# Optimization experiments

Measured on AMD Instinct MI355X. Metric: run time of the kernel, lower is better.

Reference implementation:

```python
import jax, jax.numpy as jnp
import numpy as np
import math

B, S, D, H = 16, 256, 1024, 16
DK = D // H
MAXLEN = 512


def _sinusoid_table(maxlen, dim):
    # rows for positions -maxlen .. maxlen-1  (2*maxlen rows)
    pos = jnp.arange(-maxlen, maxlen, dtype=jnp.float32)[:, None]
    i = jnp.arange(dim)
    angle = pos / jnp.power(10000.0, (2 * (i // 2)) / dim).astype(jnp.float32)
    return jnp.where(i % 2 == 0, jnp.sin(angle), jnp.cos(angle))


def setup_inputs() -> dict:
    key = jax.random.key(0)
    ks = jax.random.split(key, 13)
    std_qk = math.sqrt(2.0 / (D + DK))
    inp = {
        "x": jax.random.normal(ks[0], (B, S, D), jnp.float32),
        "Wq": jax.random.normal(ks[1], (D, D), jnp.float32) * std_qk,
        "bq": jnp.zeros((D,), jnp.float32),
        "Wk": jax.random.normal(ks[2], (D, D), jnp.float32) * std_qk,
        "bk": jnp.zeros((D,), jnp.float32),
        "Wv": jax.random.normal(ks[3], (D, D), jnp.float32) * std_qk,
        "bv": jnp.zeros((D,), jnp.float32),
        "Wr": jax.random.normal(ks[4], (D, D), jnp.float32) * std_qk,
        "br": jnp.zeros((D,), jnp.float32),
        "u_bias": jax.random.normal(ks[5], (H, DK), jnp.float32) * math.sqrt(2.0 / (H + DK)),
        "v_bias": jax.random.normal(ks[6], (H, DK), jnp.float32) * math.sqrt(2.0 / (H + DK)),
        "Wo": jax.random.normal(ks[7], (D, D), jnp.float32) * math.sqrt(2.0 / (D + D)),
        "bo": jnp.zeros((D,), jnp.float32),
    }
    return inp


def reference(x, Wq, bq, Wk, bk, Wv, bv, Wr, br, u_bias, v_bias, Wo, bo):
    table = _sinusoid_table(MAXLEN, D)  # (2*MAXLEN, D)
    # relative position indices: idx[s, z] = z - s, shifted by +MAXLEN
    relpos_idx = (jnp.arange(2 * S)[None, :] - jnp.arange(S)[:, None])[:, :S] + MAXLEN
    relpos_vec = table[relpos_idx]  # (S, S, D)

    q = (x @ Wq.T + bq).reshape(B, S, H, DK)
    k = (x @ Wk.T + bk).reshape(B, S, H, DK)
    v = (x @ Wv.T + bv).reshape(B, S, H, DK)

    rp_k = (relpos_vec @ Wk.T + bk).reshape(S, S, H, DK)       # shared k_proj
    kR = (x @ Wr.T + br).reshape(B, S, H, DK)                  # relpos_k_proj(keys)
    rp_R = (relpos_vec @ Wr.T + br).reshape(S, S, H, DK)       # relpos_k_proj(relpos)

    w = jnp.einsum('bshd,bzhd->bhsz', q, k)
    w = w + jnp.einsum('bshd,szhd->bhsz', q, rp_k)
    w = w + jnp.einsum('hd,bzhd->bhz', u_bias, kR)[:, :, None, :]
    w = w + jnp.einsum('hd,szhd->hsz', v_bias, rp_R)[None, :, :, :]
    w = w / math.sqrt(DK)

    causal = jnp.tril(jnp.ones((S, S), jnp.float32))[None, None, :, :]
    w = w + jnp.log(causal)  # -inf above diagonal

    attn = jax.nn.softmax(w, axis=-1)                          # (B,H,S,S)
    vw = jnp.einsum('bhsz,bzhd->bshd', attn, v).reshape(B, S, D)
    return vw @ Wo.T + bo
```

## Files before the change

### kernel.cpp

```cpp
#include <hip/hip_runtime.h>
#include <math.h>

constexpr int kB  = 16;
constexpr int kS  = 256;
constexpr int kD  = 1024;
constexpr int kH  = 16;
constexpr float kScale = 0.125f;

using bf16x8  = __attribute__((ext_vector_type(8))) short;
using floatx4 = __attribute__((ext_vector_type(4))) float;
typedef unsigned short u16;

__device__ __forceinline__ u16 f2bf(float x) {
  union { float f; unsigned u; } v; v.f = x;
  unsigned r = v.u + 0x7fffu + ((v.u >> 16) & 1u);
  return (u16)(r >> 16);
}
__device__ __forceinline__ float bf2f(u16 h) {
  union { unsigned u; float f; } v; v.u = ((unsigned)h) << 16;
  return v.f;
}

#define MFMA16(a, b, c) __builtin_amdgcn_mfma_f32_16x16x32_bf16((a), (b), (c), 0, 0, 0)
#define GLL16(gp, lp)                                                        \
  __builtin_amdgcn_global_load_lds(                                          \
      (const __attribute__((address_space(1))) unsigned int*)(gp),           \
      (__attribute__((address_space(3))) unsigned int*)(lp), 16, 0, 0)

__global__ __launch_bounds__(256) void pack_k(
    const float* __restrict__ x, const float* __restrict__ Wq,
    const float* __restrict__ Wk, const float* __restrict__ Wv,
    const float* __restrict__ Wo,
    const float* __restrict__ bq, const float* __restrict__ bk,
    const float* __restrict__ bv,
    const float* __restrict__ Wr, const float* __restrict__ br,
    const float* __restrict__ ub, const float* __restrict__ vb,
    u16* __restrict__ xA, u16* __restrict__ W3b, u16* __restrict__ Wob,
    float* __restrict__ b3) {
  if (blockIdx.x >= 8451) {
    int gid = (blockIdx.x - 8451) * 256 + threadIdx.x;
    int j = gid >> 10, c = gid & 1023;
    int h = j & 15;
    const float* bvec = (j < 16 ? ub : vb) + h * 64;
    const float* wcol = Wr + (size_t)(h * 64) * 1024 + c;
    float a = 0.f;
#pragma unroll
    for (int d = 0; d < 64; ++d) a += bvec[d] * wcol[(size_t)d * 1024];
    W3b[(size_t)(3072 + j) * 1024 + c] = f2bf(a);
    if (gid < 128) {
      float s = 0.f;
      if (gid < 32) {
        const float* bv2 = (gid < 16 ? ub : vb) + (gid & 15) * 64;
        const float* brp = br + (gid & 15) * 64;
        for (int d = 0; d < 64; ++d) s += bv2[d] * brp[d];
      }
      b3[3072 + gid] = s;
    }
    return;
  }
  size_t i = ((size_t)blockIdx.x * 256 + threadIdx.x) * 4;
  const size_t NX = (size_t)4194304, NW = (size_t)1048576;
  const size_t BEND = NX + 4 * NW + 3072;
  const float* src;
  u16* dst;
  size_t o;
  if (i < NX) {
    src = x; dst = xA; o = i;
  } else if (i < NX + 3 * NW) {
    size_t j = i - NX;
    int sel = (int)(j >> 20);
    o = j & (NW - 1);
    src = sel == 0 ? Wq : sel == 1 ? Wv : Wk;
    dst = W3b + (size_t)sel * NW;
  } else if (i < NX + 4 * NW) {
    o = i - NX - 3 * NW;
    src = Wo; dst = Wob;
  } else if (i < BEND) {
    size_t j = i - NX - 4 * NW;
    int sel = (int)(j >> 10);
    o = j & 1023;
    src = sel == 0 ? bq : sel == 1 ? bv : bk;
    *reinterpret_cast<float4*>(b3 + j) = *reinterpret_cast<const float4*>(src + o);
    return;
  } else if (i < BEND + 262144) {
    size_t j = i - BEND;
    int p = (int)(j >> 10);
    int ibase = (int)(j & 1023);
    ushort4 r;
    u16* rr = (u16*)&r;
#pragma unroll
    for (int c = 0; c < 4; ++c) {
      int idx = ibase + c;
      float ex = (float)(2 * (idx / 2)) * (1.0f / 1024.0f);
      float scale = exp2f(ex * -13.287712379549449f);
      float angle = (float)(p - 255) * scale;
      rr[c] = f2bf((idx & 1) ? cosf(angle) : sinf(angle));
    }
    *reinterpret_cast<ushort4*>(xA + NX + j) = r;
    return;
  } else {
    return;
  }
  float4 v = *reinterpret_cast<const float4*>(src + o);
  ushort4 r;
  r.x = f2bf(v.x); r.y = f2bf(v.y); r.z = f2bf(v.z); r.w = f2bf(v.w);
  *reinterpret_cast<ushort4*>(dst + o) = r;
}

__global__ __launch_bounds__(256) void gemm_k(
    const u16* __restrict__ A, const u16* __restrict__ W,
    const float* __restrict__ bias, float* __restrict__ Cv,
    int M, int N, int K, int mTiles, int nTiles) {
  const int xcd = blockIdx.x & 7;
  const int li  = blockIdx.x >> 3;
  const int r0   = (xcd * mTiles) >> 3;
  const int rcnt = (((xcd + 1) * mTiles) >> 3) - r0;
  if (li >= rcnt * nTiles) return;
  const int bm = (r0 + li % rcnt) * 128;
  const int bn = (li / rcnt) * 128;

  __shared__ u16 Alds[3][128 * 64];
  __shared__ u16 Blds[3][128 * 64];
  const int t = threadIdx.x, w = t >> 6, l = t & 63;
  const int l15 = l & 15, quad = l >> 4;
  const int wm = w >> 1, wn = w & 1;
  const int lrow8 = l >> 3;
  const int kslot = l & 7;
  const int NT = K >> 6;

  floatx4 acc[4][4] = {};

  auto stage = [&](int kt) {
    const int buf = kt % 3, k0 = kt << 6;
#pragma unroll
    for (int sg = 0; sg < 4; ++sg) {
      int mrow = sg * 32 + w * 8 + lrow8;
      int gk = (kslot ^ (mrow & 7)) << 3;
      GLL16(A + (size_t)(bm + mrow) * K + k0 + gk, Alds[buf] + (sg * 32 + w * 8) * 64);
      GLL16(W + (size_t)(bn + mrow) * K + k0 + gk, Blds[buf] + (sg * 32 + w * 8) * 64);
    }
  };

  stage(0); stage(1); stage(2);

  for (int kt = 0; kt < NT; ++kt) {
    if (kt + 2 < NT) {
      asm volatile("s_waitcnt vmcnt(16)" ::: "memory");
    } else if (kt + 1 < NT) {
      asm volatile("s_waitcnt vmcnt(8)" ::: "memory");
    } else {
      asm volatile("s_waitcnt vmcnt(0)" ::: "memory");
    }
    __builtin_amdgcn_s_barrier();
    __builtin_amdgcn_sched_barrier(0);
    const u16* AL = Alds[kt % 3];
    const u16* BL = Blds[kt % 3];
#pragma unroll
    for (int c = 0; c < 2; ++c) {
      bf16x8 af[4], bf[4];
#pragma unroll
      for (int mi = 0; mi < 4; ++mi) {
        int am = wm * 64 + mi * 16 + l15;
        af[mi] = *(const bf16x8*)(AL + am * 64 + (((c * 4 + quad) ^ (am & 7)) << 3));
      }
#pragma unroll
      for (int ni = 0; ni < 4; ++ni) {
        int an = wn * 64 + ni * 16 + l15;
        bf[ni] = *(const bf16x8*)(BL + an * 64 + (((c * 4 + quad) ^ (an & 7)) << 3));
      }
#pragma unroll
      for (int mi = 0; mi < 4; ++mi)
#pragma unroll
        for (int ni = 0; ni < 4; ++ni)
          acc[mi][ni] = MFMA16(af[mi], bf[ni], acc[mi][ni]);
    }
    __builtin_amdgcn_s_barrier();
    if (kt + 3 < NT) stage(kt + 3);
  }

#pragma unroll
  for (int ni = 0; ni < 4; ++ni) {
    int col = bn + wn * 64 + ni * 16 + l15;
    float bv = bias[col];
#pragma unroll
    for (int mi = 0; mi < 4; ++mi) {
      int mrow = bm + wm * 64 + mi * 16 + quad * 4;
#pragma unroll
      for (int r = 0; r < 4; ++r) {
        Cv[(size_t)(mrow + r) * N + col] = acc[mi][ni][r] + bv;
      }
    }
  }
}

__global__ __launch_bounds__(256) void gemmqvk_k(
    const u16* __restrict__ A, const u16* __restrict__ W,
    const float* __restrict__ bias, u16* __restrict__ Cv,
    int K, float* __restrict__ utb, float* __restrict__ dtb,
    int mTiles, int nTiles) {
  const int nwg = mTiles * nTiles;
  const int qq = nwg >> 3, rr8 = nwg & 7;
  const int xcd = blockIdx.x & 7;
  const int wgid = (xcd < rr8 ? xcd * (qq + 1) : rr8 * (qq + 1) + (xcd - rr8) * qq)
                   + (blockIdx.x >> 3);
  const int bm = (wgid / nTiles) * 128;
  const int bn = (wgid % nTiles) * 128;

  __shared__ u16 lds[32768];

  const int t = threadIdx.x, w = t >> 6, l = t & 63;
  const int l15 = l & 15, quad = l >> 4;
  const int wm = w >> 1, wn = w & 1;
  const int lrow8 = l >> 3;
  const int kslot = l & 7;
  const int NT = K >> 6;

  floatx4 acc[4][4] = {};

  auto stage = [&](int kt) {
    const int k0 = kt << 6;
    u16* base = lds + (kt & 1) * 16384;
#pragma unroll
    for (int sg = 0; sg < 4; ++sg) {
      int mrow = sg * 32 + w * 8 + lrow8;
      int gk = (kslot ^ (mrow & 7)) << 3;
      GLL16(A + (size_t)(bm + mrow) * K + k0 + gk, base + (sg * 32 + w * 8) * 64);
      GLL16(W + (size_t)(bn + mrow) * K + k0 + gk, base + 8192 + (sg * 32 + w * 8) * 64);
    }
  };

  stage(0);
  stage(1);

  for (int kt = 0; kt < NT; ++kt) {
    if (kt + 1 < NT) {
      asm volatile("s_waitcnt vmcnt(8)" ::: "memory");
    } else {
      asm volatile("s_waitcnt vmcnt(0)" ::: "memory");
    }
    __builtin_amdgcn_s_barrier();
    __builtin_amdgcn_sched_barrier(0);
    const u16* AL = lds + (kt & 1) * 16384;
    const u16* BL = AL + 8192;
#pragma unroll
    for (int c = 0; c < 2; ++c) {
      bf16x8 af[4], bf[4];
#pragma unroll
      for (int mi = 0; mi < 4; ++mi) {
        int am = wm * 64 + mi * 16 + l15;
        af[mi] = *(const bf16x8*)(AL + am * 64 + (((c * 4 + quad) ^ (am & 7)) << 3));
      }
#pragma unroll
      for (int ni = 0; ni < 4; ++ni) {
        int an = wn * 64 + ni * 16 + l15;
        bf[ni] = *(const bf16x8*)(BL + an * 64 + (((c * 4 + quad) ^ (an & 7)) << 3));
      }
#pragma unroll
      for (int mi = 0; mi < 4; ++mi)
#pragma unroll
        for (int ni = 0; ni < 4; ++ni)
          acc[mi][ni] = MFMA16(af[mi], bf[ni], acc[mi][ni]);
    }
    __builtin_amdgcn_s_barrier();
    if (kt + 2 < NT) stage(kt + 2);
  }

  float* fl = (float*)lds;
#pragma unroll
  for (int ni = 0; ni < 4; ++ni) {
    float bv = bias[bn + wn * 64 + ni * 16 + l15];
#pragma unroll
    for (int mi = 0; mi < 4; ++mi) {
#pragma unroll
      for (int r = 0; r < 4; ++r) {
        int lr = wm * 64 + mi * 16 + quad * 4 + r;
        int c  = wn * 64 + ni * 16 + l15;
        int key = ((r ^ quad) & 3) << 4;
        fl[lr * 128 + (c ^ key)] = acc[mi][ni][r] + bv;
      }
    }
  }
  __syncthreads();

  u16* VTp = Cv + (size_t)4194304;
  if (bn >= 1024 && bn < 2048) {
    if (bm < 4096) {
      int bb = bm >> 8;
      int zb = bm & 128;
      int c = (w & 1) * 64 + l;
      int rbase = (w >> 1) * 64;
      int col = bn + c;
      int hh2 = (col >> 6) & 15;
      u16* vpb = VTp + ((size_t)((bb << 4) + hh2) * 64 + (col & 63)) * 256 +
                 zb + rbase;
#pragma unroll 1
      for (int pp = 0; pp < 8; ++pp) {
        int rb = rbase + pp * 8;
        u16 hv[8];
#pragma unroll
        for (int e = 0; e < 8; ++e) {
          int lr = rb + e;
          int key = ((lr & 3) ^ ((lr >> 2) & 3)) << 4;
          hv[e] = f2bf(fl[lr * 128 + (c ^ key)]);
        }
        *(ushort4*)(vpb + pp * 8) = *(ushort4*)&hv[0];
        *(ushort4*)(vpb + pp * 8 + 4) = *(ushort4*)&hv[4];
      }
    }
  } else {
#pragma unroll 1
    for (int cc = 0; cc < 2; ++cc) {
      int col0 = bn + cc * 64;
#pragma unroll
      for (int rr = 0; rr < 8; ++rr) {
        int lr = w * 32 + rr * 4 + quad;
        int key = ((rr ^ quad) & 3) << 4;
        float4 v = *(const float4*)&fl[lr * 128 + ((cc * 64 + (l15 << 2)) ^ key)];
        int grow = bm + lr;
        if (col0 < 3072) {
          ushort4 hvv;
          hvv.x = f2bf(v.x); hvv.y = f2bf(v.y); hvv.z = f2bf(v.z); hvv.w = f2bf(v.w);
          int matsel = col0 >> 10;
          int hh2 = (col0 >> 6) & 15;
          if (grow < 4096) {
            int bb = grow >> 8, ss = grow & 255;
            *(ushort4*)(Cv + (size_t)matsel * 4194304 +
                        ((size_t)(((bb << 4) + hh2) << 8) + ss) * 64 + (l15 << 2)) = hvv;
          } else if (matsel == 2) {
            int pp = grow - 4096;
            *(ushort4*)(Cv + (size_t)3 * 4194304 +
                        ((size_t)((hh2 << 8) + pp)) * 64 + (l15 << 2)) = hvv;
          }
        } else if (col0 < 3104) {
#pragma unroll
          for (int e = 0; e < 4; ++e) {
            int col = col0 + (l15 << 2) + e;
            float vv = e == 0 ? v.x : e == 1 ? v.y : e == 2 ? v.z : v.w;
            if (col < 3088) {
              if (grow < 4096)
                utb[((grow >> 8) * 16 + (col - 3072)) * 256 + (grow & 255)] = vv;
            } else if (col < 3104) {
              if (grow >= 4096)
                dtb[(col - 3088) * 256 + (grow - 4096)] = vv;
            }
          }
        }
      }
    }
  }
}

__global__ __launch_bounds__(512, 2) void attn_k(
    const u16* __restrict__ Qh, const u16* __restrict__ Kh,
    const u16* __restrict__ VT, const u16* __restrict__ RPKh,
    const float* __restrict__ ut, const float* __restrict__ dt,
    u16* __restrict__ vw) {
  __shared__ float ScW[8][16 * 260];
  __shared__ float Ut[256], Dt[256];

  const int bh = blockIdx.x;
  const int h = bh & 15;
  const int b = bh >> 4;
  const size_t bh256 = (size_t)bh << 8;

  const int t = threadIdx.x, w = t >> 6, l = t & 63;
  const int l15 = l & 15, quad = l >> 4;

  if (t < 256) Ut[t] = ut[bh256 + t];
  else         Dt[t - 256] = dt[((size_t)h << 8) + (t - 256)];
  __syncthreads();

  float* scw = &ScW[w][0];

#pragma unroll 1
  for (int sidx = 0; sidx < 2; ++sidx) {
    const int s = sidx ? (15 - w) : w;
    const int rB = s << 4;

    bf16x8 qa0, qa1;
    {
      const u16* qp = Qh + (bh256 + rB + l15) * 64 + quad * 8;
      qa0 = *(const bf16x8*)qp;
      qa1 = *(const bf16x8*)(qp + 32);
    }
    bf16x8 kA0, kA1, kB0, kB1, rA0, rA1, rB0, rB1;
    {
      const u16* kp = Kh + (bh256 + l15) * 64 + quad * 8;
      kA0 = *(const bf16x8*)kp;
      kA1 = *(const bf16x8*)(kp + 32);
      const u16* rp = RPKh + (((size_t)h << 8) + 240 - rB + l15) * 64 + quad * 8;
      rA0 = *(const bf16x8*)rp;
      rA1 = *(const bf16x8*)(rp + 32);
    }

#pragma unroll
    for (int j = 0; j < 16; ++j) {
      if (j > s) break;
      if (j + 1 <= s) {
        const u16* kp = Kh + (bh256 + ((j + 1) << 4) + l15) * 64 + quad * 8;
        const u16* rp = RPKh + (((size_t)h << 8) + 240 - rB + ((j + 1) << 4) + l15) * 64 + quad * 8;
        if ((j + 1) & 1) {
          kB0 = *(const bf16x8*)kp; kB1 = *(const bf16x8*)(kp + 32);
          rB0 = *(const bf16x8*)rp; rB1 = *(const bf16x8*)(rp + 32);
        } else {
          kA0 = *(const bf16x8*)kp; kA1 = *(const bf16x8*)(kp + 32);
          rA0 = *(const bf16x8*)rp; rA1 = *(const bf16x8*)(rp + 32);
        }
      }
      bf16x8 k0 = (j & 1) ? kB0 : kA0;
      bf16x8 k1 = (j & 1) ? kB1 : kA1;
      bf16x8 r0 = (j & 1) ? rB0 : rA0;
      bf16x8 r1 = (j & 1) ? rB1 : rA1;
      {
        floatx4 acc = {};
        acc = MFMA16(qa0, k0, acc);
        acc = MFMA16(qa1, k1, acc);
        float u = Ut[(j << 4) + l15];
#pragma unroll
        for (int r = 0; r < 4; ++r)
          scw[(4 * quad + r) * 260 + (j << 4) + l15] = acc[r] + u;
      }
      {
        floatx4 acc = {};
        acc = MFMA16(qa0, r0, acc);
        acc = MFMA16(qa1, r1, acc);
        float dv = Dt[240 - rB + (j << 4) + l15];
#pragma unroll
        for (int r = 0; r < 4; ++r) {
          int z = (j << 4) + l15 + 4 * quad + r - 15;
          if (z >= 0)
            scw[(4 * quad + r) * 260 + z] += acc[r] + dv;
        }
      }
    }

    const int kcmax = s >> 1;
    const int Rabs = rB + l15;
    float m = -1e30f;
#pragma unroll
    for (int kc = 0; kc < 8; ++kc) {
      if (kc > kcmax) break;
      const float* sp = scw + l15 * 260 + kc * 32 + quad * 8;
      floatx4 v0 = *(const floatx4*)sp;
      floatx4 v1 = *(const floatx4*)(sp + 4);
#pragma unroll
      for (int e = 0; e < 4; ++e) {
        int z = kc * 32 + quad * 8 + e;
        if (z <= Rabs) m = fmaxf(m, v0[e]);
        if (z + 4 <= Rabs) m = fmaxf(m, v1[e]);
      }
    }
    m = fmaxf(m, __shfl_xor(m, 16));
    m = fmaxf(m, __shfl_xor(m, 32));
    m *= kScale;

    floatx4 oacc[4] = {};
    float sum = 0.f;
    bf16x8 vA[4], vB[4];
    {
      const u16* vp = VT + ((size_t)bh * 64 + l15) * 256 + quad * 8;
#pragma unroll
      for (int nt = 0; nt < 4; ++nt)
        vA[nt] = *(const bf16x8*)(vp + (size_t)nt * 16 * 256);
    }
#pragma unroll
    for (int kc = 0; kc < 8; ++kc) {
      if (kc > kcmax) break;
      if (kc + 1 <= kcmax) {
        const u16* vp = VT + ((size_t)bh * 64 + l15) * 256 + (kc + 1) * 32 + quad * 8;
        if ((kc + 1) & 1) {
#pragma unroll
          for (int nt = 0; nt < 4; ++nt)
            vB[nt] = *(const bf16x8*)(vp + (size_t)nt * 16 * 256);
        } else {
#pragma unroll
          for (int nt = 0; nt < 4; ++nt)
            vA[nt] = *(const bf16x8*)(vp + (size_t)nt * 16 * 256);
        }
      }
      const float* sp = scw + l15 * 260 + kc * 32 + quad * 8;
      floatx4 v0 = *(const floatx4*)sp;
      floatx4 v1 = *(const floatx4*)(sp + 4);
      bf16x8 pa;
#pragma unroll
      for (int e = 0; e < 4; ++e) {
        int z = kc * 32 + quad * 8 + e;
        float p0 = (z <= Rabs) ? __expf(v0[e] * kScale - m) : 0.f;
        float p1 = (z + 4 <= Rabs) ? __expf(v1[e] * kScale - m) : 0.f;
        sum += p0 + p1;
        pa[e] = (short)f2bf(p0);
        pa[e + 4] = (short)f2bf(p1);
      }
#pragma unroll
      for (int nt = 0; nt < 4; ++nt)
        oacc[nt] = MFMA16(pa, (kc & 1) ? vB[nt] : vA[nt], oacc[nt]);
    }
    sum += __shfl_xor(sum, 16);
    sum += __shfl_xor(sum, 32);
    float rinv = 1.f / sum;

#pragma unroll
    for (int r = 0; r < 4; ++r) {
      float rs = __shfl(rinv, 4 * quad + r);
      int row = rB + 4 * quad + r;
#pragma unroll
      for (int nt = 0; nt < 4; ++nt)
        vw[(size_t)(b * 256 + row) * 1024 + h * 64 + nt * 16 + l15] =
            f2bf(oacc[nt][r] * rs);
    }
  }
}

extern "C" void kernel_launch(void* const* d_in, const int* in_sizes, int n_in,
                              void* d_out, int out_size, void* d_ws, size_t ws_size,
                              hipStream_t stream) {
  const float* x  = (const float*)d_in[0];
  const float* Wq = (const float*)d_in[1];
  const float* bq = (const float*)d_in[2];
  const float* Wk = (const float*)d_in[3];
  const float* bk = (const float*)d_in[4];
  const float* Wv = (const float*)d_in[5];
  const float* bv = (const float*)d_in[6];
  const float* Wr = (const float*)d_in[7];
  const float* br = (const float*)d_in[8];
  const float* ub = (const float*)d_in[9];
  const float* vb = (const float*)d_in[10];
  const float* Wo = (const float*)d_in[11];
  const float* bo = (const float*)d_in[12];
  float* out = (float*)d_out;

  char* base = (char*)d_ws;
  size_t off = 0;
  auto alloc = [&](size_t bytes) {
    void* p = base + off;
    off += (bytes + 255) & ~(size_t)255;
    return p;
  };

  const size_t MAT = (size_t)4194304;
  u16*   xA    = (u16*)alloc((size_t)4352 * 1024 * 2);
  u16*   W3b   = (u16*)alloc((size_t)3328 * 1024 * 2);
  u16*   Wob   = (u16*)alloc((size_t)1024 * 1024 * 2);
  float* b3    = (float*)alloc((size_t)3328 * 4);
  u16*   Ph    = (u16*)alloc((3 * MAT + 262144) * 2);
  float* utb   = (float*)alloc((size_t)65536 * 4);
  float* dtb   = (float*)alloc((size_t)4096 * 4);
  u16*   vwb   = (u16*)alloc((size_t)4096 * 1024 * 2);

  u16* Qh   = Ph;
  u16* VTb  = Ph + MAT;
  u16* Kh   = Ph + 2 * MAT;
  u16* RPKh = Ph + 3 * MAT;

  pack_k<<<dim3(8579), dim3(256), 0, stream>>>(x, Wq, Wk, Wv, Wo, bq, bk, bv,
                                               Wr, br, ub, vb,
                                               xA, W3b, Wob, b3);

  gemmqvk_k<<<dim3(884), dim3(256), 0, stream>>>(xA, W3b, b3, Ph,
                                                 1024, utb, dtb, 34, 26);

  attn_k<<<dim3(256), dim3(512), 0, stream>>>(Qh, Kh, VTb, RPKh, utb, dtb, vwb);

  gemm_k<<<dim3(256), dim3(256), 0, stream>>>(vwb, Wob, bo, out,
                                              4096, 1024, 1024, 32, 8);
}
```

Measured before the change: 187.4 us.

## Load A fragments directly from global, halve LDS, raise QKV GEMM occupancy

The QKV projection GEMM now reads A-operand fragments straight from global memory into registers, and stages only the W tile through LDS. This halves shared memory to 32 KB and allows a launch bound of 3 workgroups per CU. The epilogue transposes the output tile in two 64-row halves so it fits in the smaller LDS buffer. The grid also drops one column tile that did no useful work. The trade-off is that A is no longer shared through LDS: both wn waves fetch the same A rows from global/L2, and those row-strided loads are less coalesced and may stall the MFMA loop.

```diff
diff --git a/kernel.cpp b/kernel.cpp
--- a/kernel.cpp
+++ b/kernel.cpp
@@ -193,7 +193,7 @@
   }
 }
 
-__global__ __launch_bounds__(256) void gemmqvk_k(
+__global__ __launch_bounds__(256, 3) void gemmqvk_k(
     const u16* __restrict__ A, const u16* __restrict__ W,
     const float* __restrict__ bias, u16* __restrict__ Cv,
     int K, float* __restrict__ utb, float* __restrict__ dtb,
@@ -206,7 +206,7 @@
   const int bm = (wgid / nTiles) * 128;
   const int bn = (wgid % nTiles) * 128;
 
-  __shared__ u16 lds[32768];
+  __shared__ u16 lds[2 * 8192];
 
   const int t = threadIdx.x, w = t >> 6, l = t & 63;
   const int l15 = l & 15, quad = l >> 4;
@@ -217,39 +217,40 @@
 
   floatx4 acc[4][4] = {};
 
-  auto stage = [&](int kt) {
+  auto stageB = [&](int kt) {
     const int k0 = kt << 6;
-    u16* base = lds + (kt & 1) * 16384;
+    u16* base = lds + (kt & 1) * 8192;
 #pragma unroll
     for (int sg = 0; sg < 4; ++sg) {
       int mrow = sg * 32 + w * 8 + lrow8;
       int gk = (kslot ^ (mrow & 7)) << 3;
-      GLL16(A + (size_t)(bm + mrow) * K + k0 + gk, base + (sg * 32 + w * 8) * 64);
-      GLL16(W + (size_t)(bn + mrow) * K + k0 + gk, base + 8192 + (sg * 32 + w * 8) * 64);
+      GLL16(W + (size_t)(bn + mrow) * K + k0 + gk, base + (sg * 32 + w * 8) * 64);
     }
   };
 
-  stage(0);
-  stage(1);
+  stageB(0);
 
   for (int kt = 0; kt < NT; ++kt) {
+    const int k0 = kt << 6;
+    bf16x8 af[2][4];
+#pragma unroll
+    for (int c = 0; c < 2; ++c)
+#pragma unroll
+      for (int mi = 0; mi < 4; ++mi)
+        af[c][mi] = *(const bf16x8*)(A +
+            (size_t)(bm + wm * 64 + mi * 16 + l15) * K + k0 + c * 32 + quad * 8);
     if (kt + 1 < NT) {
+      stageB(kt + 1);
+      asm volatile("s_waitcnt vmcnt(12)" ::: "memory");
+    } else {
       asm volatile("s_waitcnt vmcnt(8)" ::: "memory");
-    } else {
-      asm volatile("s_waitcnt vmcnt(0)" ::: "memory");
     }
     __builtin_amdgcn_s_barrier();
     __builtin_amdgcn_sched_barrier(0);
-    const u16* AL = lds + (kt & 1) * 16384;
-    const u16* BL = AL + 8192;
+    const u16* BL = lds + (kt & 1) * 8192;
 #pragma unroll
     for (int c = 0; c < 2; ++c) {
-      bf16x8 af[4], bf[4];
-#pragma unroll
-      for (int mi = 0; mi < 4; ++mi) {
-        int am = wm * 64 + mi * 16 + l15;
-        af[mi] = *(const bf16x8*)(AL + am * 64 + (((c * 4 + quad) ^ (am & 7)) << 3));
-      }
+      bf16x8 bf[4];
 #pragma unroll
       for (int ni = 0; ni < 4; ++ni) {
         int an = wn * 64 + ni * 16 + l15;
@@ -259,89 +260,93 @@
       for (int mi = 0; mi < 4; ++mi)
 #pragma unroll
         for (int ni = 0; ni < 4; ++ni)
-          acc[mi][ni] = MFMA16(af[mi], bf[ni], acc[mi][ni]);
+          acc[mi][ni] = MFMA16(af[c][mi], bf[ni], acc[mi][ni]);
     }
     __builtin_amdgcn_s_barrier();
-    if (kt + 2 < NT) stage(kt + 2);
   }
 
   float* fl = (float*)lds;
-#pragma unroll
-  for (int ni = 0; ni < 4; ++ni) {
-    float bv = bias[bn + wn * 64 + ni * 16 + l15];
-#pragma unroll
-    for (int mi = 0; mi < 4; ++mi) {
-#pragma unroll
-      for (int r = 0; r < 4; ++r) {
-        int lr = wm * 64 + mi * 16 + quad * 4 + r;
-        int c  = wn * 64 + ni * 16 + l15;
-        int key = ((r ^ quad) & 3) << 4;
-        fl[lr * 128 + (c ^ key)] = acc[mi][ni][r] + bv;
-      }
-    }
-  }
-  __syncthreads();
-
   u16* VTp = Cv + (size_t)4194304;
-  if (bn >= 1024 && bn < 2048) {
-    if (bm < 4096) {
-      int bb = bm >> 8;
-      int zb = bm & 128;
-      int c = (w & 1) * 64 + l;
-      int rbase = (w >> 1) * 64;
-      int col = bn + c;
-      int hh2 = (col >> 6) & 15;
-      u16* vpb = VTp + ((size_t)((bb << 4) + hh2) * 64 + (col & 63)) * 256 +
-                 zb + rbase;
 #pragma unroll 1
-      for (int pp = 0; pp < 8; ++pp) {
-        int rb = rbase + pp * 8;
-        u16 hv[8];
-#pragma unroll
-        for (int e = 0; e < 8; ++e) {
-          int lr = rb + e;
-          int key = ((lr & 3) ^ ((lr >> 2) & 3)) << 4;
-          hv[e] = f2bf(fl[lr * 128 + (c ^ key)]);
+  for (int hh = 0; hh < 2; ++hh) {
+    __syncthreads();
+    if (wm == hh) {
+#pragma unroll
+      for (int ni = 0; ni < 4; ++ni) {
+        float bv = bias[bn + wn * 64 + ni * 16 + l15];
+#pragma unroll
+        for (int mi = 0; mi < 4; ++mi) {
+#pragma unroll
+          for (int r = 0; r < 4; ++r) {
+            int lr = mi * 16 + quad * 4 + r;
+            int c  = wn * 64 + ni * 16 + l15;
+            int key = ((r ^ quad) & 3) << 4;
+            fl[lr * 128 + (c ^ key)] = acc[mi][ni][r] + bv;
+          }
         }
-        *(ushort4*)(vpb + pp * 8) = *(ushort4*)&hv[0];
-        *(ushort4*)(vpb + pp * 8 + 4) = *(ushort4*)&hv[4];
-      }
-    }
-  } else {
+      }
+    }
+    __syncthreads();
+    if (bn >= 1024 && bn < 2048) {
+      if (bm < 4096) {
+        int bb = bm >> 8;
+        int zb = bm & 128;
+        int c = (w & 1) * 64 + l;
+        int rbase = (w >> 1) * 32;
+        int col = bn + c;
+        int hh2 = (col >> 6) & 15;
+        u16* vpb = VTp + ((size_t)((bb << 4) + hh2) * 64 + (col & 63)) * 256 +
+                   zb + hh * 64 + rbase;
 #pragma unroll 1
-    for (int cc = 0; cc < 2; ++cc) {
-      int col0 = bn + cc * 64;
-#pragma unroll
-      for (int rr = 0; rr < 8; ++rr) {
-        int lr = w * 32 + rr * 4 + quad;
-        int key = ((rr ^ quad) & 3) << 4;
-        float4 v = *(const float4*)&fl[lr * 128 + ((cc * 64 + (l15 << 2)) ^ key)];
-        int grow = bm + lr;
-        if (col0 < 3072) {
-          ushort4 hvv;
-          hvv.x = f2bf(v.x); hvv.y = f2bf(v.y); hvv.z = f2bf(v.z); hvv.w = f2bf(v.w);
-          int matsel = col0 >> 10;
-          int hh2 = (col0 >> 6) & 15;
-          if (grow < 4096) {
-            int bb = grow >> 8, ss = grow & 255;
-            *(ushort4*)(Cv + (size_t)matsel * 4194304 +
-                        ((size_t)(((bb << 4) + hh2) << 8) + ss) * 64 + (l15 << 2)) = hvv;
-          } else if (matsel == 2) {
-            int pp = grow - 4096;
-            *(ushort4*)(Cv + (size_t)3 * 4194304 +
-                        ((size_t)((hh2 << 8) + pp)) * 64 + (l15 << 2)) = hvv;
+        for (int pp = 0; pp < 4; ++pp) {
+          int rb = rbase + pp * 8;
+          u16 hv[8];
+#pragma unroll
+          for (int e = 0; e < 8; ++e) {
+            int lr = rb + e;
+            int key = ((lr & 3) ^ ((lr >> 2) & 3)) << 4;
+            hv[e] = f2bf(fl[lr * 128 + (c ^ key)]);
           }
-        } else if (col0 < 3104) {
-#pragma unroll
-          for (int e = 0; e < 4; ++e) {
-            int col = col0 + (l15 << 2) + e;
-            float vv = e == 0 ? v.x : e == 1 ? v.y : e == 2 ? v.z : v.w;
-            if (col < 3088) {
-              if (grow < 4096)
-                utb[((grow >> 8) * 16 + (col - 3072)) * 256 + (grow & 255)] = vv;
-            } else if (col < 3104) {
-              if (grow >= 4096)
-                dtb[(col - 3088) * 256 + (grow - 4096)] = vv;
+          *(ushort4*)(vpb + pp * 8) = *(ushort4*)&hv[0];
+          *(ushort4*)(vpb + pp * 8 + 4) = *(ushort4*)&hv[4];
+        }
+      }
+    } else {
+#pragma unroll 1
+      for (int cc = 0; cc < 2; ++cc) {
+        int col0 = bn + cc * 64;
+#pragma unroll
+        for (int rr = 0; rr < 4; ++rr) {
+          int lr = w * 16 + rr * 4 + quad;
+          int key = ((rr ^ quad) & 3) << 4;
+          float4 v = *(const float4*)&fl[lr * 128 + ((cc * 64 + (l15 << 2)) ^ key)];
+          int grow = bm + hh * 64 + lr;
+          if (col0 < 3072) {
+            ushort4 hvv;
+            hvv.x = f2bf(v.x); hvv.y = f2bf(v.y); hvv.z = f2bf(v.z); hvv.w = f2bf(v.w);
+            int matsel = col0 >> 10;
+            int hh3 = (col0 >> 6) & 15;
+            if (grow < 4096) {
+              int bb = grow >> 8, ss = grow & 255;
+              *(ushort4*)(Cv + (size_t)matsel * 4194304 +
+                          ((size_t)(((bb << 4) + hh3) << 8) + ss) * 64 + (l15 << 2)) = hvv;
+            } else if (matsel == 2) {
+              int pp = grow - 4096;
+              *(ushort4*)(Cv + (size_t)3 * 4194304 +
+                          ((size_t)((hh3 << 8) + pp)) * 64 + (l15 << 2)) = hvv;
+            }
+          } else if (col0 < 3104) {
+#pragma unroll
+            for (int e = 0; e < 4; ++e) {
+              int col = col0 + (l15 << 2) + e;
+              float vv = e == 0 ? v.x : e == 1 ? v.y : e == 2 ? v.z : v.w;
+              if (col < 3088) {
+                if (grow < 4096)
+                  utb[((grow >> 8) * 16 + (col - 3072)) * 256 + (grow & 255)] = vv;
+              } else if (col < 3104) {
+                if (grow >= 4096)
+                  dtb[(col - 3088) * 256 + (grow - 4096)] = vv;
+              }
             }
           }
         }
@@ -556,8 +561,8 @@
                                                Wr, br, ub, vb,
                                                xA, W3b, Wob, b3);
 
-  gemmqvk_k<<<dim3(884), dim3(256), 0, stream>>>(xA, W3b, b3, Ph,
-                                                 1024, utb, dtb, 34, 26);
+  gemmqvk_k<<<dim3(850), dim3(256), 0, stream>>>(xA, W3b, b3, Ph,
+                                                 1024, utb, dtb, 34, 25);
 
   attn_k<<<dim3(256), dim3(512), 0, stream>>>(Qh, Kh, VTb, RPKh, utb, dtb, vwb);
 
```

New measurement: 225.6 us. 1.2x slower.
